# Kernel tuning notes

Measured on AMD Instinct MI355X. Metric: run time of the kernel, lower is better.

## Reference

```python
import jax, jax.numpy as jnp
import numpy as np

B, H, W, C, NBHD, T, OUT_DIM = 4, 96, 96, 256, 48, 3025, 512
N = H * W
INNER = 4
DS_RATE = 0.25


def _layer_norm(x, w, b, eps=1e-5):
    mu = jnp.mean(x, axis=-1, keepdims=True)
    var = jnp.mean((x - mu) ** 2, axis=-1, keepdims=True)
    return (x - mu) * jax.lax.rsqrt(var + eps) * w + b


def setup_inputs() -> dict:
    key = jax.random.key(0)
    ks = jax.random.split(key, 8)
    # regular grid positions: pos % 4 == 0 (both dims) on exactly 24*24=576 tokens
    yy, xx = jnp.meshgrid(jnp.arange(H), jnp.arange(W), indexing='ij')
    pos = jnp.stack([yy, xx], axis=-1).reshape(1, N, 2).astype(jnp.float32)
    pos = jnp.broadcast_to(pos, (B, N, 2))
    feat = jax.random.normal(ks[0], (B, N, C), dtype=jnp.float32)
    member_idx = jax.random.randint(ks[1], (B, N, NBHD), 0, N)
    cluster_mask = (jax.random.uniform(ks[2], (B, N, NBHD)) > 0.1).astype(jnp.float32)
    learned_prob = jax.random.uniform(ks[3], (B, N, 1), dtype=jnp.float32)
    pe_idx = jax.random.randint(ks[4], (B, N, NBHD), 0, T)
    pre_table = jax.random.normal(ks[5], (T, 5), dtype=jnp.float32)
    # weight_net: Linear(5,4) + LayerNorm(4) + GELU
    w1 = jax.random.normal(ks[6], (5, INNER), dtype=jnp.float32) * 0.3
    b1 = jnp.zeros((INNER,), jnp.float32)
    ln1_w = jnp.ones((INNER,), jnp.float32)
    ln1_b = jnp.zeros((INNER,), jnp.float32)
    # norm over inner_ch*dim, then Linear(inner_ch*dim -> out_dim)
    norm_w = jnp.ones((INNER * C,), jnp.float32)
    norm_b = jnp.zeros((INNER * C,), jnp.float32)
    lin_w = jax.random.normal(ks[7], (INNER * C, OUT_DIM), dtype=jnp.float32) * 0.02
    lin_b = jnp.zeros((OUT_DIM,), jnp.float32)
    return {
        'pos': pos, 'feat': feat, 'member_idx': member_idx,
        'cluster_mask': cluster_mask, 'learned_prob': learned_prob,
        'pe_idx': pe_idx, 'pre_table': pre_table,
        'w1': w1, 'b1': b1, 'ln1_w': ln1_w, 'ln1_b': ln1_b,
        'norm_w': norm_w, 'norm_b': norm_b, 'lin_w': lin_w, 'lin_b': lin_b,
        'stride': 2, 'reserve_num': 576,
    }


def reference(pos, feat, member_idx, cluster_mask, learned_prob, pe_idx,
              pre_table, w1, b1, ln1_w, ln1_b, norm_w, norm_b, lin_w, lin_b,
              stride, reserve_num):
    b, n, c = feat.shape
    nbhd = member_idx.shape[-1]
    keep_num = int(n * DS_RATE)
    sample_num = keep_num - reserve_num

    pos_long = pos.astype(jnp.int32)
    lp_det = jax.lax.stop_gradient(learned_prob[..., 0])  # b x n (detached in torch)
    reserve_mask = jnp.all(pos_long % (stride * 2) == 0, axis=-1).astype(jnp.float32)
    final_prob = lp_det + reserve_mask * (-100.0)

    # topk sampled tokens (reserved tokens pushed to -100 so never sampled)
    sample_idx = jax.lax.top_k(final_prob, sample_num)[1]  # b x sample_num
    # reserved token indices in ascending index order (torch nonzero order)
    reserve_idx = jnp.argsort(-reserve_mask, axis=1, stable=True)[:, :reserve_num]
    idx = jnp.concatenate([sample_idx, reserve_idx], axis=1)  # b x keep_num

    pos_down = jnp.take_along_axis(pos, idx[:, :, None], axis=1)  # b x keep x 2

    member_d = jnp.take_along_axis(member_idx, idx[:, :, None], axis=1)   # b x keep x nbhd
    pe_d = jnp.take_along_axis(pe_idx, idx[:, :, None], axis=1)
    cmask_d = jnp.take_along_axis(cluster_mask, idx[:, :, None], axis=1)

    flat_mi = member_d.reshape(b, keep_num * nbhd)
    # gather learned prob of each neighbor (NOT detached: grads flow)
    lp_nb = jnp.take_along_axis(learned_prob, flat_mi[:, :, None], axis=1)
    lp_nb = lp_nb.reshape(b, keep_num, nbhd, 1)

    # weight_net over pre-computed position table -> T x inner_ch
    wt = jax.nn.gelu(_layer_norm(pre_table @ w1 + b1, ln1_w, ln1_b))
    weights = wt[pe_d]  # b x keep x nbhd x inner_ch
    weights = weights * (lp_nb * cmask_d[..., None])

    # gather neighbor features and do position-weighted aggregation
    feat_g = jnp.take_along_axis(feat, flat_mi[:, :, None], axis=1)
    feat_g = feat_g.reshape(b, keep_num, nbhd, c)
    feat_down = jnp.einsum('bnkm,bnkc->bnmc', weights, feat_g)
    feat_down = feat_down.reshape(b, keep_num, INNER * c)

    feat_down = _layer_norm(feat_down, norm_w, norm_b)
    feat_down = feat_down @ lin_w + lin_b
    return pos_down, feat_down
```

## Files before the change

### kernel.cpp

```cpp
#include <hip/hip_runtime.h>
#include <hip/hip_bf16.h>
#include <stdint.h>

#define BB 4
#define NN 9216
#define CC 256
#define NBHD 48
#define T_TAB 3025
#define OUT_DIM 512
#define KEEP 2304
#define RESERVE 576
#define SAMPLE 1728
#define W_IMG 96
#define CAND_CAP 6144

typedef __attribute__((ext_vector_type(4))) float f32x4;
typedef __attribute__((ext_vector_type(8))) short s16x8;

__device__ inline unsigned short f2bf_bits(float x) {
    __hip_bfloat16 h = __float2bfloat16(x);
    return __builtin_bit_cast(unsigned short, h);
}

__device__ inline unsigned int fkey(float v) {
    unsigned int u = __builtin_bit_cast(unsigned int, v);
    return (u & 0x80000000u) ? ~u : (u | 0x80000000u);
}
__device__ inline float final_prob_val(const float* lpb, int i) {
    int y = i / W_IMG, x = i % W_IMG;
    bool res = ((y & 3) == 0) && ((x & 3) == 0);
    return lpb[i] + (res ? -100.0f : 0.0f);
}

__global__ __launch_bounds__(256) void prep_kernel(
        const float* __restrict__ W, __hip_bfloat16* __restrict__ Wt,
        const float* __restrict__ pre_table,
        const float* __restrict__ w1, const float* __restrict__ b1,
        const float* __restrict__ ln1w, const float* __restrict__ ln1b,
        float* __restrict__ wt,
        const float* __restrict__ lp, int* __restrict__ hist,
        const float* __restrict__ feat, unsigned short* __restrict__ featb) {
    if (blockIdx.x < 512) {
        __shared__ float s[32][33];
        int bx = blockIdx.x & 15;
        int by = blockIdx.x >> 4;
        int tx = threadIdx.x & 31, ty = threadIdx.x >> 5;
#pragma unroll
        for (int r = 0; r < 4; r++)
            s[ty * 4 + r][tx] = W[(size_t)(by * 32 + ty * 4 + r) * 512 + bx * 32 + tx];
        __syncthreads();
#pragma unroll
        for (int r = 0; r < 4; r++)
            Wt[(size_t)(bx * 32 + ty * 4 + r) * 1024 + by * 32 + tx] =
                __float2bfloat16(s[tx][ty * 4 + r]);
        return;
    }
    if (blockIdx.x < 524) {
        int t = (blockIdx.x - 512) * 256 + threadIdx.x;
        if (t >= T_TAB) return;
        float p[5];
#pragma unroll
        for (int j = 0; j < 5; j++) p[j] = pre_table[t * 5 + j];
        float h[4];
#pragma unroll
        for (int m = 0; m < 4; m++) {
            float a = b1[m];
#pragma unroll
            for (int j = 0; j < 5; j++) a += p[j] * w1[j * 4 + m];
            h[m] = a;
        }
        float mu = 0.25f * (h[0] + h[1] + h[2] + h[3]);
        float var = 0.f;
#pragma unroll
        for (int m = 0; m < 4; m++) { float d = h[m] - mu; var += d * d; }
        var *= 0.25f;
        float rs = rsqrtf(var + 1e-5f);
#pragma unroll
        for (int m = 0; m < 4; m++) {
            float x = (h[m] - mu) * rs * ln1w[m] + ln1b[m];
            float u = 0.7978845608028654f * (x + 0.044715f * x * x * x);
            wt[t * 4 + m] = 0.5f * x * (1.0f + tanhf(u));
        }
        return;
    }
    if (blockIdx.x < 668) {
        int g = (blockIdx.x - 524) * 256 + threadIdx.x;
        int b = g / NN, i = g % NN;
        float v = final_prob_val(lp + b * NN, i);
        unsigned int bin = fkey(v) >> 16;
        atomicAdd(&hist[b * 65536 + bin], 1);
        return;
    }
    {
        int g = (blockIdx.x - 668) * 256 + threadIdx.x;
        float4 v = ((const float4*)feat)[g];
        ushort4 u;
        u.x = f2bf_bits(v.x); u.y = f2bf_bits(v.y);
        u.z = f2bf_bits(v.z); u.w = f2bf_bits(v.w);
        ((ushort4*)featb)[g] = u;
    }
}

__global__ __launch_bounds__(256) void thresh_kernel(const int* __restrict__ hist,
                                                     int* __restrict__ thr) {
    int b = blockIdx.x, t = threadIdx.x;
    __shared__ int s_scan[256];
    __shared__ int s_rc, s_ex;
    const int* h = hist + b * 65536;
    int lo = 65536 - (t + 1) * 256;
    const int4* h4 = (const int4*)(h + lo);
    int sum = 0;
#pragma unroll 8
    for (int k = 0; k < 64; k++) {
        int4 v = h4[k];
        sum += v.x + v.y + v.z + v.w;
    }
    int own = sum;
    s_scan[t] = sum;
    __syncthreads();
    for (int off = 1; off < 256; off <<= 1) {
        int add = (t >= off) ? s_scan[t - off] : 0;
        __syncthreads();
        s_scan[t] += add;
        __syncthreads();
    }
    int incl = s_scan[t], ex = incl - own;
    if (ex < SAMPLE && incl >= SAMPLE) { s_rc = t; s_ex = ex; }
    __syncthreads();
    int rc = s_rc, ex0 = s_ex;
    int bin = 65536 - rc * 256 - 1 - t;
    int own2 = h[bin];
    s_scan[t] = own2;
    __syncthreads();
    for (int off = 1; off < 256; off <<= 1) {
        int add = (t >= off) ? s_scan[t - off] : 0;
        __syncthreads();
        s_scan[t] += add;
        __syncthreads();
    }
    int incl2 = ex0 + s_scan[t], ex2 = incl2 - own2;
    if (ex2 < SAMPLE && incl2 >= SAMPLE) thr[b] = bin;
}

__global__ __launch_bounds__(256) void collect_kernel(
        const float* __restrict__ lp,
        const int* __restrict__ thr,
        int* __restrict__ cnt,
        unsigned long long* __restrict__ candk,
        int* __restrict__ idx,
        float* __restrict__ pos_down) {
    __shared__ int s_wcnt[4];
    __shared__ int s_base;
    int g = blockIdx.x * 256 + threadIdx.x;
    int b = g / NN, i = g % NN;
    int lane = threadIdx.x & 63, wave = threadIdx.x >> 6;
    int y = i / W_IMG, x = i % W_IMG;
    bool res = ((y & 3) == 0) && ((x & 3) == 0);
    float v = lp[g];
    bool pred = false;
    if (res) {
        int slot = SAMPLE + (y >> 2) * (W_IMG / 4) + (x >> 2);
        idx[b * KEEP + slot] = i;
        pos_down[(b * KEEP + slot) * 2 + 0] = (float)y;
        pos_down[(b * KEEP + slot) * 2 + 1] = (float)x;
    } else {
        pred = ((int)(fkey(v) >> 16) >= thr[b]);
    }
    unsigned long long m = __ballot(pred);
    int wcount = __popcll(m);
    int lpos = __popcll(m & ((1ull << lane) - 1ull));
    if (lane == 0) s_wcnt[wave] = wcount;
    __syncthreads();
    if (threadIdx.x == 0) {
        int tot = s_wcnt[0] + s_wcnt[1] + s_wcnt[2] + s_wcnt[3];
        s_base = atomicAdd(&cnt[b], tot);
    }
    __syncthreads();
    if (pred) {
        int off = s_base + lpos;
        for (int w = 0; w < wave; w++) off += s_wcnt[w];
        if (off < CAND_CAP)
            candk[b * CAND_CAP + off] =
                ((unsigned long long)fkey(v) << 32) | (unsigned int)(NN - 1 - i);
    }
}

#define RCHUNK 2048
__global__ __launch_bounds__(256) void rank_cand_kernel(
        const int* __restrict__ cnt,
        const unsigned long long* __restrict__ candk,
        int* __restrict__ idx,
        float* __restrict__ pos_down) {
    __shared__ unsigned long long sk[RCHUNK];
    int b = blockIdx.y;
    int C = cnt[b]; if (C > CAND_CAP) C = CAND_CAP;
    if ((int)(blockIdx.x * 256) >= C) return;
    int i = blockIdx.x * 256 + threadIdx.x;
    bool valid = (i < C);
    unsigned long long ki = valid ? candk[b * CAND_CAP + i] : 0ull;
    int rank = 0;
    for (int base = 0; base < C; base += RCHUNK) {
        int len = min(RCHUNK, C - base);
        for (int j = threadIdx.x; j < len; j += 256)
            sk[j] = candk[b * CAND_CAP + base + j];
        __syncthreads();
        if (valid) {
            int j = 0;
            for (; j + 16 <= len; j += 16) {
#pragma unroll
                for (int u = 0; u < 16; u++)
                    rank += (int)(sk[j + u] > ki);
            }
            for (; j < len; j++) rank += (int)(sk[j] > ki);
        }
        __syncthreads();
    }
    if (valid && rank < SAMPLE) {
        int ii = NN - 1 - (int)(ki & 0xffffffffULL);
        idx[b * KEEP + rank] = ii;
        pos_down[(b * KEEP + rank) * 2 + 0] = (float)(ii / W_IMG);
        pos_down[(b * KEEP + rank) * 2 + 1] = (float)(ii % W_IMG);
    }
}

#define ASTRIDE 20
__global__ __launch_bounds__(256) void agg_kernel(
        const __hip_bfloat16* __restrict__ feat,
        const int* __restrict__ member_idx,
        const float* __restrict__ cmask,
        const float* __restrict__ lp,
        const int* __restrict__ pe_idx,
        const float* __restrict__ wt,
        const int* __restrict__ idx,
        const float* __restrict__ norm_w,
        const float* __restrict__ norm_b,
        __hip_bfloat16* __restrict__ xnorm) {
    int L = blockIdx.x;
    int b = (L >> 1) & 3;
    int t = (L >> 3) * 2 + (L & 1);
    int tid = threadIdx.x;
    __shared__ int s_mem[NBHD];
    __shared__ float s_w[NBHD * 4];
    __shared__ float s_part[4 * 64 * ASTRIDE];
    __shared__ float s_red[8];
    int i = idx[b * KEEP + t];
    if (tid < NBHD) {
        size_t base = ((size_t)b * NN + i) * NBHD + tid;
        int mi = member_idx[base];
        int pe = pe_idx[base];
        float fsc = lp[b * NN + mi] * cmask[base];
        s_mem[tid] = mi;
        s_w[tid * 4 + 0] = wt[pe * 4 + 0] * fsc;
        s_w[tid * 4 + 1] = wt[pe * 4 + 1] * fsc;
        s_w[tid * 4 + 2] = wt[pe * 4 + 2] * fsc;
        s_w[tid * 4 + 3] = wt[pe * 4 + 3] * fsc;
    }
    __syncthreads();
    int wave = tid >> 6, lane = tid & 63;
    const __hip_bfloat16* fbase = feat + (size_t)b * NN * CC;
    float acc[4][4] = {};
#pragma unroll
    for (int j = 0; j < 12; j++) {
        int k = wave * 12 + j;
        int mi = s_mem[k];
        float4 w4 = *(const float4*)&s_w[k * 4];
        uint2 v = *((const uint2*)(fbase + (size_t)mi * CC) + lane);
        float f0 = __builtin_bit_cast(float, v.x << 16);
        float f1 = __builtin_bit_cast(float, v.x & 0xffff0000u);
        float f2 = __builtin_bit_cast(float, v.y << 16);
        float f3 = __builtin_bit_cast(float, v.y & 0xffff0000u);
        acc[0][0] += w4.x * f0; acc[0][1] += w4.x * f1; acc[0][2] += w4.x * f2; acc[0][3] += w4.x * f3;
        acc[1][0] += w4.y * f0; acc[1][1] += w4.y * f1; acc[1][2] += w4.y * f2; acc[1][3] += w4.y * f3;
        acc[2][0] += w4.z * f0; acc[2][1] += w4.z * f1; acc[2][2] += w4.z * f2; acc[2][3] += w4.z * f3;
        acc[3][0] += w4.w * f0; acc[3][1] += w4.w * f1; acc[3][2] += w4.w * f2; acc[3][3] += w4.w * f3;
    }
    float* pp = &s_part[(wave * 64 + lane) * ASTRIDE];
#pragma unroll
    for (int m = 0; m < 4; m++)
        *(float4*)(pp + m * 4) = make_float4(acc[m][0], acc[m][1], acc[m][2], acc[m][3]);
    __syncthreads();
    int cl = tid >> 2, cc = tid & 3;
    float a0 = 0.f, a1 = 0.f, a2 = 0.f, a3 = 0.f;
#pragma unroll
    for (int w = 0; w < 4; w++) {
        const float* q = &s_part[(w * 64 + cl) * ASTRIDE + cc];
        a0 += q[0]; a1 += q[4]; a2 += q[8]; a3 += q[12];
    }
    float s1 = a0 + a1 + a2 + a3;
    float s2 = a0 * a0 + a1 * a1 + a2 * a2 + a3 * a3;
    for (int off = 32; off > 0; off >>= 1) {
        s1 += __shfl_down(s1, off);
        s2 += __shfl_down(s2, off);
    }
    int wid = tid >> 6;
    if ((tid & 63) == 0) { s_red[wid] = s1; s_red[4 + wid] = s2; }
    __syncthreads();
    float S1 = s_red[0] + s_red[1] + s_red[2] + s_red[3];
    float S2 = s_red[4] + s_red[5] + s_red[6] + s_red[7];
    float mu = S1 * (1.0f / 1024.0f);
    float var = S2 * (1.0f / 1024.0f) - mu * mu;
    float rs = rsqrtf(var + 1e-5f);
    __hip_bfloat16* xo = xnorm + ((size_t)(b * KEEP + t)) * 1024;
    xo[0 * 256 + tid] = __float2bfloat16((a0 - mu) * rs * norm_w[0 * 256 + tid] + norm_b[0 * 256 + tid]);
    xo[1 * 256 + tid] = __float2bfloat16((a1 - mu) * rs * norm_w[1 * 256 + tid] + norm_b[1 * 256 + tid]);
    xo[2 * 256 + tid] = __float2bfloat16((a2 - mu) * rs * norm_w[2 * 256 + tid] + norm_b[2 * 256 + tid]);
    xo[3 * 256 + tid] = __float2bfloat16((a3 - mu) * rs * norm_w[3 * 256 + tid] + norm_b[3 * 256 + tid]);
}

__device__ inline void async16(const void* g, void* l) {
    __builtin_amdgcn_global_load_lds(
        (const __attribute__((address_space(1))) void*)g,
        (__attribute__((address_space(3))) void*)l, 16, 0, 0);
}
__device__ inline void mfma16x16x32(f32x4& d, const s16x8& a, const s16x8& b) {
    asm("v_mfma_f32_16x16x32_bf16 %0, %1, %2, %0" : "+v"(d) : "v"(a), "v"(b));
}

__global__ __launch_bounds__(256) void mfma_gemm(
        const __hip_bfloat16* __restrict__ A,
        const __hip_bfloat16* __restrict__ Bt,
        const float* __restrict__ bias,
        float* __restrict__ Cout) {
    __shared__ __hip_bfloat16 sA[128 * 32];
    __shared__ __hip_bfloat16 sB[128 * 32];
    int tid = threadIdx.x;
    int wave = tid >> 6, lane = tid & 63;
    int wm = wave >> 1, wn = wave & 1;
    int row0 = blockIdx.y * 128, col0 = blockIdx.x * 128;

    int lrow = lane >> 2;
    int lcol = (lane & 3) * 8;
    const __hip_bfloat16* gA = A + (size_t)(row0 + wave * 32 + lrow) * 1024 + lcol;
    const __hip_bfloat16* gB = Bt + (size_t)(col0 + wave * 32 + lrow) * 1024 + lcol;
    __hip_bfloat16* lA0 = sA + (wave * 32) * 32;
    __hip_bfloat16* lA1 = sA + (wave * 32 + 16) * 32;
    __hip_bfloat16* lB0 = sB + (wave * 32) * 32;
    __hip_bfloat16* lB1 = sB + (wave * 32 + 16) * 32;

    f32x4 acc[4][4] = {};
    int fr = lane & 15;
    int fq = lane >> 4;

    for (int kk = 0; kk < 1024; kk += 32) {
        async16(gA + kk, lA0);
        async16(gA + kk + 16 * 1024, lA1);
        async16(gB + kk, lB0);
        async16(gB + kk + 16 * 1024, lB1);
        __syncthreads();
        s16x8 af[4], bf[4];
#pragma unroll
        for (int i = 0; i < 4; i++)
            af[i] = *(const s16x8*)(sA + (wm * 64 + i * 16 + fr) * 32 + fq * 8);
#pragma unroll
        for (int j = 0; j < 4; j++)
            bf[j] = *(const s16x8*)(sB + (wn * 64 + j * 16 + fr) * 32 + fq * 8);
#pragma unroll
        for (int i = 0; i < 4; i++)
#pragma unroll
            for (int j = 0; j < 4; j++)
                mfma16x16x32(acc[i][j], af[i], bf[j]);
        __syncthreads();
    }
    asm volatile("s_nop 7\ns_nop 7" ::);
    float bv[4];
#pragma unroll
    for (int j = 0; j < 4; j++) bv[j] = bias[col0 + wn * 64 + j * 16 + fr];
#pragma unroll
    for (int i = 0; i < 4; i++) {
        int row = row0 + wm * 64 + i * 16 + fq * 4;
#pragma unroll
        for (int j = 0; j < 4; j++) {
            int col = col0 + wn * 64 + j * 16 + fr;
            float* cp = Cout + (size_t)row * 512 + col;
#pragma unroll
            for (int r = 0; r < 4; r++)
                cp[(size_t)r * 512] = acc[i][j][r] + bv[j];
        }
    }
}

extern "C" void kernel_launch(void* const* d_in, const int* in_sizes, int n_in,
                              void* d_out, int out_size, void* d_ws, size_t ws_size,
                              hipStream_t stream) {
    const float* pos       = (const float*)d_in[0];
    const float* feat      = (const float*)d_in[1];
    const int*   member_idx= (const int*)d_in[2];
    const float* cmask     = (const float*)d_in[3];
    const float* lp        = (const float*)d_in[4];
    const int*   pe_idx    = (const int*)d_in[5];
    const float* pre_table = (const float*)d_in[6];
    const float* w1        = (const float*)d_in[7];
    const float* b1        = (const float*)d_in[8];
    const float* ln1w      = (const float*)d_in[9];
    const float* ln1b      = (const float*)d_in[10];
    const float* norm_w    = (const float*)d_in[11];
    const float* norm_b    = (const float*)d_in[12];
    const float* lin_w     = (const float*)d_in[13];
    const float* lin_b     = (const float*)d_in[14];

    float* out = (float*)d_out;
    float* pos_down = out;
    float* feat_out = out + (size_t)BB * KEEP * 2;

    char* ws = (char*)d_ws;
    float*              wt     = (float*)(ws + 0);
    int*                hist   = (int*)  (ws + 48640);
    int*                ccnt   = (int*)  (ws + 1097216);
    int*                thr    = (int*)  (ws + 1097472);
    unsigned long long* candk  = (unsigned long long*)(ws + 1097728);
    int*                idx    = (int*)  (ws + 1294336);
    __hip_bfloat16*     wtb    = (__hip_bfloat16*)(ws + 1331200);
    __hip_bfloat16*     xnormb = (__hip_bfloat16*)(ws + 2379776);
    __hip_bfloat16*     featb  = (__hip_bfloat16*)(ws + 21254144);

    hipMemsetAsync(hist, 0, 1048576 + 256, stream);
    prep_kernel<<<dim3(512 + 12 + 144 + (BB * NN * CC / 4) / 256), 256, 0, stream>>>(
        lin_w, wtb, pre_table, w1, b1, ln1w, ln1b, wt, lp, hist,
        feat, (unsigned short*)featb);
    thresh_kernel<<<dim3(BB), 256, 0, stream>>>(hist, thr);
    collect_kernel<<<dim3((BB * NN) / 256), 256, 0, stream>>>(lp, thr, ccnt, candk, idx, pos_down);
    rank_cand_kernel<<<dim3(CAND_CAP / 256, BB), 256, 0, stream>>>(ccnt, candk, idx, pos_down);
    agg_kernel<<<dim3(BB * KEEP), 256, 0, stream>>>(
        featb, member_idx, cmask, lp, pe_idx, wt, idx, norm_w, norm_b, xnormb);
    mfma_gemm<<<dim3(OUT_DIM / 128, (BB * KEEP) / 128), 256, 0, stream>>>(xnormb, wtb, lin_b, feat_out);
}
```

Baseline: 227.9 us.

## Assign one wave per output token in aggregation kernel, drop block syncs

The aggregation kernel now maps each wavefront to one kept token, so a block handles four tokens instead of one. Each half-wave covers alternate neighbours and loads 16-byte feature chunks. Partial sums are combined and LayerNorm statistics reduced with cross-lane shuffles instead of shared-memory partials and __syncthreads. This removes block barriers and LDS traffic and widens the loads, but each lane holds more accumulator registers and half the lanes sit idle during the final store.

```diff
diff --git a/kernel.cpp b/kernel.cpp
--- a/kernel.cpp
+++ b/kernel.cpp
@@ -223,9 +223,8 @@
     }
 }
 
-#define ASTRIDE 20
 __global__ __launch_bounds__(256) void agg_kernel(
-        const __hip_bfloat16* __restrict__ feat,
+        const unsigned short* __restrict__ featb,
         const int* __restrict__ member_idx,
         const float* __restrict__ cmask,
         const float* __restrict__ lp,
@@ -235,76 +234,89 @@
         const float* __restrict__ norm_w,
         const float* __restrict__ norm_b,
         __hip_bfloat16* __restrict__ xnorm) {
+    __shared__ int   s_mi[4][64];
+    __shared__ float s_w4[4][192];
+    int tid = threadIdx.x, wave = tid >> 6, lane = tid & 63;
     int L = blockIdx.x;
     int b = (L >> 1) & 3;
-    int t = (L >> 3) * 2 + (L & 1);
-    int tid = threadIdx.x;
-    __shared__ int s_mem[NBHD];
-    __shared__ float s_w[NBHD * 4];
-    __shared__ float s_part[4 * 64 * ASTRIDE];
-    __shared__ float s_red[8];
+    int t = (((L >> 3) * 2 + (L & 1)) << 2) + wave;
     int i = idx[b * KEEP + t];
-    if (tid < NBHD) {
-        size_t base = ((size_t)b * NN + i) * NBHD + tid;
+    if (lane < NBHD) {
+        size_t base = ((size_t)b * NN + i) * NBHD + lane;
         int mi = member_idx[base];
         int pe = pe_idx[base];
         float fsc = lp[b * NN + mi] * cmask[base];
-        s_mem[tid] = mi;
-        s_w[tid * 4 + 0] = wt[pe * 4 + 0] * fsc;
-        s_w[tid * 4 + 1] = wt[pe * 4 + 1] * fsc;
-        s_w[tid * 4 + 2] = wt[pe * 4 + 2] * fsc;
-        s_w[tid * 4 + 3] = wt[pe * 4 + 3] * fsc;
-    }
-    __syncthreads();
-    int wave = tid >> 6, lane = tid & 63;
-    const __hip_bfloat16* fbase = feat + (size_t)b * NN * CC;
-    float acc[4][4] = {};
-#pragma unroll
-    for (int j = 0; j < 12; j++) {
-        int k = wave * 12 + j;
-        int mi = s_mem[k];
-        float4 w4 = *(const float4*)&s_w[k * 4];
-        uint2 v = *((const uint2*)(fbase + (size_t)mi * CC) + lane);
-        float f0 = __builtin_bit_cast(float, v.x << 16);
-        float f1 = __builtin_bit_cast(float, v.x & 0xffff0000u);
-        float f2 = __builtin_bit_cast(float, v.y << 16);
-        float f3 = __builtin_bit_cast(float, v.y & 0xffff0000u);
-        acc[0][0] += w4.x * f0; acc[0][1] += w4.x * f1; acc[0][2] += w4.x * f2; acc[0][3] += w4.x * f3;
-        acc[1][0] += w4.y * f0; acc[1][1] += w4.y * f1; acc[1][2] += w4.y * f2; acc[1][3] += w4.y * f3;
-        acc[2][0] += w4.z * f0; acc[2][1] += w4.z * f1; acc[2][2] += w4.z * f2; acc[2][3] += w4.z * f3;
-        acc[3][0] += w4.w * f0; acc[3][1] += w4.w * f1; acc[3][2] += w4.w * f2; acc[3][3] += w4.w * f3;
-    }
-    float* pp = &s_part[(wave * 64 + lane) * ASTRIDE];
+        s_mi[wave][lane] = mi;
+        float4 w4 = *(const float4*)&wt[pe * 4];
+        w4.x *= fsc; w4.y *= fsc; w4.z *= fsc; w4.w *= fsc;
+        *(float4*)&s_w4[wave][lane * 4] = w4;
+    }
+    asm volatile("s_waitcnt lgkmcnt(0)" ::: "memory");
+
+    int h = lane >> 5, ln = lane & 31;
+    const unsigned short* fb = featb + (size_t)b * NN * CC + ln * 8;
+    float acc[4][8] = {};
+#pragma unroll 4
+    for (int j = 0; j < 24; j++) {
+        int k = j * 2 + h;
+        int mi = s_mi[wave][k];
+        float4 w4 = *(const float4*)&s_w4[wave][k * 4];
+        uint4 v = *(const uint4*)(fb + (size_t)mi * CC);
+        float f[8];
+        f[0] = __builtin_bit_cast(float, v.x << 16);
+        f[1] = __builtin_bit_cast(float, v.x & 0xffff0000u);
+        f[2] = __builtin_bit_cast(float, v.y << 16);
+        f[3] = __builtin_bit_cast(float, v.y & 0xffff0000u);
+        f[4] = __builtin_bit_cast(float, v.z << 16);
+        f[5] = __builtin_bit_cast(float, v.z & 0xffff0000u);
+        f[6] = __builtin_bit_cast(float, v.w << 16);
+        f[7] = __builtin_bit_cast(float, v.w & 0xffff0000u);
+#pragma unroll
+        for (int c = 0; c < 8; c++) {
+            acc[0][c] += w4.x * f[c];
+            acc[1][c] += w4.y * f[c];
+            acc[2][c] += w4.z * f[c];
+            acc[3][c] += w4.w * f[c];
+        }
+    }
 #pragma unroll
     for (int m = 0; m < 4; m++)
-        *(float4*)(pp + m * 4) = make_float4(acc[m][0], acc[m][1], acc[m][2], acc[m][3]);
-    __syncthreads();
-    int cl = tid >> 2, cc = tid & 3;
-    float a0 = 0.f, a1 = 0.f, a2 = 0.f, a3 = 0.f;
-#pragma unroll
-    for (int w = 0; w < 4; w++) {
-        const float* q = &s_part[(w * 64 + cl) * ASTRIDE + cc];
-        a0 += q[0]; a1 += q[4]; a2 += q[8]; a3 += q[12];
-    }
-    float s1 = a0 + a1 + a2 + a3;
-    float s2 = a0 * a0 + a1 * a1 + a2 * a2 + a3 * a3;
-    for (int off = 32; off > 0; off >>= 1) {
-        s1 += __shfl_down(s1, off);
-        s2 += __shfl_down(s2, off);
-    }
-    int wid = tid >> 6;
-    if ((tid & 63) == 0) { s_red[wid] = s1; s_red[4 + wid] = s2; }
-    __syncthreads();
-    float S1 = s_red[0] + s_red[1] + s_red[2] + s_red[3];
-    float S2 = s_red[4] + s_red[5] + s_red[6] + s_red[7];
-    float mu = S1 * (1.0f / 1024.0f);
-    float var = S2 * (1.0f / 1024.0f) - mu * mu;
+#pragma unroll
+        for (int c = 0; c < 8; c++)
+            acc[m][c] += __shfl_xor(acc[m][c], 32);
+    float s1 = 0.f, s2 = 0.f;
+#pragma unroll
+    for (int m = 0; m < 4; m++)
+#pragma unroll
+        for (int c = 0; c < 8; c++) { float a = acc[m][c]; s1 += a; s2 += a * a; }
+#pragma unroll
+    for (int off = 1; off < 32; off <<= 1) {
+        s1 += __shfl_xor(s1, off);
+        s2 += __shfl_xor(s2, off);
+    }
+    float mu = s1 * (1.0f / 1024.0f);
+    float var = s2 * (1.0f / 1024.0f) - mu * mu;
     float rs = rsqrtf(var + 1e-5f);
-    __hip_bfloat16* xo = xnorm + ((size_t)(b * KEEP + t)) * 1024;
-    xo[0 * 256 + tid] = __float2bfloat16((a0 - mu) * rs * norm_w[0 * 256 + tid] + norm_b[0 * 256 + tid]);
-    xo[1 * 256 + tid] = __float2bfloat16((a1 - mu) * rs * norm_w[1 * 256 + tid] + norm_b[1 * 256 + tid]);
-    xo[2 * 256 + tid] = __float2bfloat16((a2 - mu) * rs * norm_w[2 * 256 + tid] + norm_b[2 * 256 + tid]);
-    xo[3 * 256 + tid] = __float2bfloat16((a3 - mu) * rs * norm_w[3 * 256 + tid] + norm_b[3 * 256 + tid]);
+    if (h == 0) {
+        __hip_bfloat16* xo = xnorm + (size_t)(b * KEEP + t) * 1024 + ln * 8;
+#pragma unroll
+        for (int m = 0; m < 4; m++) {
+            const float* nw = norm_w + m * 256 + ln * 8;
+            const float* nb = norm_b + m * 256 + ln * 8;
+            float4 w0 = *(const float4*)nw, w1 = *(const float4*)(nw + 4);
+            float4 b0 = *(const float4*)nb, b1 = *(const float4*)(nb + 4);
+            unsigned short us[8];
+            us[0] = f2bf_bits((acc[m][0] - mu) * rs * w0.x + b0.x);
+            us[1] = f2bf_bits((acc[m][1] - mu) * rs * w0.y + b0.y);
+            us[2] = f2bf_bits((acc[m][2] - mu) * rs * w0.z + b0.z);
+            us[3] = f2bf_bits((acc[m][3] - mu) * rs * w0.w + b0.w);
+            us[4] = f2bf_bits((acc[m][4] - mu) * rs * w1.x + b1.x);
+            us[5] = f2bf_bits((acc[m][5] - mu) * rs * w1.y + b1.y);
+            us[6] = f2bf_bits((acc[m][6] - mu) * rs * w1.z + b1.z);
+            us[7] = f2bf_bits((acc[m][7] - mu) * rs * w1.w + b1.w);
+            *(uint4*)(xo + m * 256) = *(const uint4*)us;
+        }
+    }
 }
 
 __device__ inline void async16(const void* g, void* l) {
@@ -420,7 +432,8 @@
     thresh_kernel<<<dim3(BB), 256, 0, stream>>>(hist, thr);
     collect_kernel<<<dim3((BB * NN) / 256), 256, 0, stream>>>(lp, thr, ccnt, candk, idx, pos_down);
     rank_cand_kernel<<<dim3(CAND_CAP / 256, BB), 256, 0, stream>>>(ccnt, candk, idx, pos_down);
-    agg_kernel<<<dim3(BB * KEEP), 256, 0, stream>>>(
-        featb, member_idx, cmask, lp, pe_idx, wt, idx, norm_w, norm_b, xnormb);
+    agg_kernel<<<dim3((BB * KEEP) / 4), 256, 0, stream>>>(
+        (const unsigned short*)featb, member_idx, cmask, lp, pe_idx, wt, idx,
+        norm_w, norm_b, xnormb);
     mfma_gemm<<<dim3(OUT_DIM / 128, (BB * KEEP) / 128), 256, 0, stream>>>(xnormb, wtb, lin_b, feat_out);
 }
```

Result: faster. 218.5 us (-4.1%).
